# Performance work log

Hardware: AMD Instinct MI355X
Metric: run time of the kernel (lower is better)

The kernel has to match this reference:

```python
import jax, jax.numpy as jnp
import numpy as np

B, T, C, H = 2, 2048, 1024, 16
D = C // H  # head_dim = 64

def setup_inputs() -> dict:
    key = jax.random.key(0)
    ks = jax.random.split(key, 5)
    x = jax.random.normal(ks[0], (B, T, C), dtype=jnp.float32)
    Wqkv = jax.random.normal(ks[1], (C, 3 * C), dtype=jnp.float32) * 0.02
    bqkv = jnp.zeros((3 * C,), dtype=jnp.float32)
    Wout = jax.random.normal(ks[2], (C, C), dtype=jnp.float32) * 0.02
    bout = jnp.zeros((C,), dtype=jnp.float32)
    return {"x": x, "Wqkv": Wqkv, "bqkv": bqkv, "Wout": Wout, "bout": bout}

def reference(x, Wqkv, bqkv, Wout, bout):
    Bb, Tt, Cc = x.shape
    qkv = x @ Wqkv + bqkv                       # [B,T,3C]
    qkv = qkv.reshape(Bb, Tt, 3, H, D)
    qkv = jnp.transpose(qkv, (2, 0, 3, 1, 4))   # [3,B,H,T,D]
    q, k, v = qkv[0], qkv[1], qkv[2]
    scale = 1.0 / np.sqrt(D).astype(np.float32)
    scores = jnp.einsum('bhqd,bhkd->bhqk', q, k) * scale  # [B,H,T,T]
    causal = jnp.tril(jnp.ones((Tt, Tt), dtype=bool))
    scores = jnp.where(causal[None, None, :, :], scores, jnp.float32(-jnp.inf))
    attn = jax.nn.softmax(scores, axis=-1)
    out = jnp.einsum('bhqk,bhkd->bhqd', attn, v)          # [B,H,T,D]
    out = jnp.transpose(out, (0, 2, 1, 3)).reshape(Bb, Tt, Cc)
    return out @ Wout + bout
```

## Files before the change

### kernel.cpp

```cpp
#include <hip/hip_runtime.h>

#define Bc 2
#define Tc 2048
#define Cc 1024
#define Hc 16
#define Dc 64
#define Mtot (Bc*Tc)
#define Kdim Cc
#define N1 (3*Cc)
#define N2 Cc

typedef __attribute__((ext_vector_type(8))) short short8;
typedef __attribute__((ext_vector_type(4))) float float4v;

__device__ __forceinline__ unsigned short f2bf(float f) {
  unsigned int u = __builtin_bit_cast(unsigned int, f);
  u += 0x7FFFu + ((u >> 16) & 1u);
  return (unsigned short)(u >> 16);
}

__device__ __forceinline__ unsigned int pk_bf16(float a, float b) {
#if __has_builtin(__builtin_amdgcn_cvt_pk_bf16_f32)
  typedef __attribute__((ext_vector_type(2))) __bf16 bf16x2;
  bf16x2 v = __builtin_amdgcn_cvt_pk_bf16_f32(a, b);
  return __builtin_bit_cast(unsigned int, v);
#else
  return (unsigned int)f2bf(a) | ((unsigned int)f2bf(b) << 16);
#endif
}

__device__ __forceinline__ void gl2lds16(const unsigned short* g, unsigned short* l) {
  __builtin_amdgcn_global_load_lds((const __attribute__((address_space(1))) void*)g,
                                   (__attribute__((address_space(3))) void*)l, 16, 0, 0);
}

__global__ __launch_bounds__(256) void k_cvt_x(const float* __restrict__ x,
                                               unsigned short* __restrict__ xb, int n4) {
  int i = blockIdx.x * 256 + threadIdx.x;
  if (i >= n4) return;
  float4 v = ((const float4*)x)[i];
  uint2 o;
  o.x = pk_bf16(v.x, v.y);
  o.y = pk_bf16(v.z, v.w);
  ((uint2*)xb)[i] = o;
}

__global__ __launch_bounds__(256) void k_cvt_wT(const float* __restrict__ w,
                                                unsigned short* __restrict__ wT,
                                                int K, int N) {
  __shared__ float tile[32][33];
  int n0 = blockIdx.x * 32, k0 = blockIdx.y * 32;
  int tx = threadIdx.x & 31, ty = threadIdx.x >> 5;
  for (int i = 0; i < 4; ++i)
    tile[ty + 8*i][tx] = w[(size_t)(k0 + ty + 8*i) * N + n0 + tx];
  __syncthreads();
  for (int i = 0; i < 4; ++i)
    wT[(size_t)(n0 + ty + 8*i) * K + k0 + tx] = f2bf(tile[tx][ty + 8*i]);
}

__device__ __forceinline__ void gemm_mainloop(const unsigned short* __restrict__ A,
                                              const unsigned short* __restrict__ BT,
                                              int m0, int n0,
                                              unsigned short* As, unsigned short* Bs,
                                              float4v acc[4][4]) {
  const int tid = threadIdx.x;
  const int w = tid >> 6, lane = tid & 63;
  const int ln = lane & 15, qd = lane >> 4;
  const int wm = w >> 1, wn = w & 1;
  const int c0 = tid, c1 = tid + 256;
  const int row0 = c0 >> 2, ko0 = (c0 & 3) * 8;
  const int row1 = c1 >> 2, ko1 = (c1 & 3) * 8;
  for (int kk = 0; kk < Kdim; kk += 32) {
    __syncthreads();
    gl2lds16(A  + (size_t)(m0 + row0) * Kdim + kk + ko0, As + c0 * 8);
    gl2lds16(A  + (size_t)(m0 + row1) * Kdim + kk + ko1, As + c1 * 8);
    gl2lds16(BT + (size_t)(n0 + row0) * Kdim + kk + ko0, Bs + c0 * 8);
    gl2lds16(BT + (size_t)(n0 + row1) * Kdim + kk + ko1, Bs + c1 * 8);
    __syncthreads();
    short8 af[4], bf[4];
    for (int i = 0; i < 4; ++i)
      af[i] = *(const short8*)(As + (wm*64 + i*16 + ln) * 32 + qd*8);
    for (int j = 0; j < 4; ++j)
      bf[j] = *(const short8*)(Bs + (wn*64 + j*16 + ln) * 32 + qd*8);
    for (int i = 0; i < 4; ++i)
      for (int j = 0; j < 4; ++j)
        acc[i][j] = __builtin_amdgcn_mfma_f32_16x16x32_bf16(af[i], bf[j], acc[i][j], 0, 0, 0);
  }
}

__global__ __launch_bounds__(256) void k_gemm_qkv(const unsigned short* __restrict__ A,
                                                  const unsigned short* __restrict__ BT,
                                                  const float* __restrict__ bias,
                                                  unsigned short* __restrict__ qkv) {
  __shared__ alignas(16) unsigned short smem[64*136 + 64];
  unsigned short* As = smem;
  unsigned short* Bs = smem + 4096;
  const int m0 = blockIdx.y * 128, n0 = blockIdx.x * 128;
  const float4v zero4 = {0.f, 0.f, 0.f, 0.f};
  float4v acc[4][4];
  for (int i = 0; i < 4; ++i) for (int j = 0; j < 4; ++j) acc[i][j] = zero4;
  gemm_mainloop(A, BT, m0, n0, As, Bs, acc);
  const int tid = threadIdx.x;
  const int w = tid >> 6, lane = tid & 63;
  const int ln = lane & 15, qd = lane >> 4;
  const int wm = w >> 1, wn = w & 1;
  const int s = n0 >> 10;
  if (s < 2) {
    const float scale = (s == 0) ? 0.125f : 1.0f;
    for (int i = 0; i < 4; ++i) {
      int mbase = m0 + wm*64 + i*16 + qd*4;
      for (int j = 0; j < 4; ++j) {
        int ncol = n0 + wn*64 + j*16 + ln;
        float bv = bias[ncol];
        int rem = ncol & 1023;
        int h = rem >> 6, d = rem & 63;
        for (int r = 0; r < 4; ++r) {
          int m = mbase + r;
          int b = m >> 11, t = m & 2047;
          float val = (acc[i][j][r] + bv) * scale;
          qkv[((((size_t)s*Bc + b)*Hc + h)*Tc + t)*Dc + d] = f2bf(val);
        }
      }
    }
  } else {
    unsigned short* vbase = qkv + (size_t)2*Bc*Hc*Tc*Dc;
    const int b = m0 >> 11, t0 = m0 & 2047;
    const int h0 = (n0 & 1023) >> 6;
    for (int p = 0; p < 2; ++p) {
      __syncthreads();
      if (wn == p) {
        for (int i = 0; i < 4; ++i) {
          int tl = wm*64 + i*16 + qd*4;
          for (int j = 0; j < 4; ++j) {
            int dl = j*16 + ln;
            float bv = bias[n0 + p*64 + dl];
            uint2 pk;
            pk.x = pk_bf16(acc[i][j][0] + bv, acc[i][j][1] + bv);
            pk.y = pk_bf16(acc[i][j][2] + bv, acc[i][j][3] + bv);
            *(uint2*)(smem + dl*136 + tl) = pk;
          }
        }
      }
      __syncthreads();
      for (int ii = 0; ii < 4; ++ii) {
        int idx = tid + 256*ii;
        int row = idx >> 4, c16 = idx & 15;
        int4 v = *(const int4*)(smem + row*136 + c16*8);
        *(int4*)(vbase + (((size_t)b*Hc + h0 + p)*Dc + row)*Tc + t0 + c16*8) = v;
      }
    }
  }
}

__global__ __launch_bounds__(256) void k_gemm_out(const unsigned short* __restrict__ A,
                                                  const unsigned short* __restrict__ BT,
                                                  const float* __restrict__ bias,
                                                  float* __restrict__ out) {
  __shared__ alignas(16) unsigned short As[64*32];
  __shared__ alignas(16) unsigned short Bs[128*32];
  const int m0 = blockIdx.y * 64, n0 = blockIdx.x * 128;
  const int tid = threadIdx.x;
  const int w = tid >> 6, lane = tid & 63;
  const int ln = lane & 15, qd = lane >> 4;
  const int wm = w >> 1, wn = w & 1;
  const int arow = tid >> 2, ako = (tid & 3) * 8;
  const int c0 = tid, c1 = tid + 256;
  const int brow0 = c0 >> 2, bko0 = (c0 & 3) * 8;
  const int brow1 = c1 >> 2, bko1 = (c1 & 3) * 8;
  const float4v zero4 = {0.f, 0.f, 0.f, 0.f};
  float4v acc[2][4];
  for (int i = 0; i < 2; ++i) for (int j = 0; j < 4; ++j) acc[i][j] = zero4;
  for (int kk = 0; kk < Kdim; kk += 32) {
    __syncthreads();
    gl2lds16(A  + (size_t)(m0 + arow)  * Kdim + kk + ako,  As + tid * 8);
    gl2lds16(BT + (size_t)(n0 + brow0) * Kdim + kk + bko0, Bs + c0 * 8);
    gl2lds16(BT + (size_t)(n0 + brow1) * Kdim + kk + bko1, Bs + c1 * 8);
    __syncthreads();
    short8 af[2], bf[4];
    for (int i = 0; i < 2; ++i)
      af[i] = *(const short8*)(As + (wm*32 + i*16 + ln) * 32 + qd*8);
    for (int j = 0; j < 4; ++j)
      bf[j] = *(const short8*)(Bs + (wn*64 + j*16 + ln) * 32 + qd*8);
    for (int i = 0; i < 2; ++i)
      for (int j = 0; j < 4; ++j)
        acc[i][j] = __builtin_amdgcn_mfma_f32_16x16x32_bf16(af[i], bf[j], acc[i][j], 0, 0, 0);
  }
  for (int i = 0; i < 2; ++i) {
    int mbase = m0 + wm*32 + i*16 + qd*4;
    for (int j = 0; j < 4; ++j) {
      int ncol = n0 + wn*64 + j*16 + ln;
      float bv = bias[ncol];
      for (int r = 0; r < 4; ++r)
        out[(size_t)(mbase + r) * N2 + ncol] = acc[i][j][r] + bv;
    }
  }
}

__device__ __forceinline__ void attn_substep(
    const unsigned short* __restrict__ Ks, const unsigned short* __restrict__ Vt,
    unsigned short* __restrict__ pw,
    const short8 qa0, const short8 qa1,
    float4v* o, float& m_i, float& l_i,
    int k0, int myq, bool mask, int ln, int qd)
{
  const float L2E = 1.44269504f;
  const float4v zero4 = {0.f, 0.f, 0.f, 0.f};
  float4v s[4];
  for (int ki = 0; ki < 4; ++ki) {
    s[ki] = zero4;
    const unsigned short* kr = Ks + (ki*16 + ln)*72;
    short8 kf0 = *(const short8*)(kr + qd*8);
    short8 kf1 = *(const short8*)(kr + 32 + qd*8);
    s[ki] = __builtin_amdgcn_mfma_f32_16x16x32_bf16(kf0, qa0, s[ki], 0, 0, 0);
    s[ki] = __builtin_amdgcn_mfma_f32_16x16x32_bf16(kf1, qa1, s[ki], 0, 0, 0);
  }
  if (mask) {
    for (int ki = 0; ki < 4; ++ki) {
      int key = k0 + ki*16 + qd*4;
      for (int r = 0; r < 4; ++r)
        if (key + r > myq) s[ki][r] = -1e30f;
    }
  }
  float mt = -1e30f;
  for (int ki = 0; ki < 4; ++ki)
    for (int r = 0; r < 4; ++r) mt = fmaxf(mt, s[ki][r]);
  mt = fmaxf(mt, __shfl_xor(mt, 16));
  mt = fmaxf(mt, __shfl_xor(mt, 32));
  float mn = fmaxf(m_i, mt);
  float al = exp2f((m_i - mn) * L2E);
  m_i = mn;
  float st = 0.f;
  for (int ki = 0; ki < 4; ++ki)
    for (int r = 0; r < 4; ++r) {
      s[ki][r] = exp2f((s[ki][r] - mn) * L2E);
      st += s[ki][r];
    }
  st += __shfl_xor(st, 16);
  st += __shfl_xor(st, 32);
  l_i = l_i * al + st;
  for (int dt = 0; dt < 4; ++dt)
    for (int r = 0; r < 4; ++r) o[dt][r] *= al;
  for (int ki = 0; ki < 4; ++ki) {
    uint2 p2;
    p2.x = pk_bf16(s[ki][0], s[ki][1]);
    p2.y = pk_bf16(s[ki][2], s[ki][3]);
    *(uint2*)(pw + ln*72 + ki*16 + qd*4) = p2;
  }
  short8 pb0 = *(const short8*)(pw + ln*72 + qd*8);
  short8 pb1 = *(const short8*)(pw + ln*72 + 32 + qd*8);
  for (int dt = 0; dt < 4; ++dt) {
    const unsigned short* vr = Vt + (dt*16 + ln)*72;
    short8 va0 = *(const short8*)(vr + qd*8);
    short8 va1 = *(const short8*)(vr + 32 + qd*8);
    o[dt] = __builtin_amdgcn_mfma_f32_16x16x32_bf16(va0, pb0, o[dt], 0, 0, 0);
    o[dt] = __builtin_amdgcn_mfma_f32_16x16x32_bf16(va1, pb1, o[dt], 0, 0, 0);
  }
}

__global__ __launch_bounds__(256) void k_attn(const unsigned short* __restrict__ qb,
                                              const unsigned short* __restrict__ kb,
                                              const unsigned short* __restrict__ vT,
                                              unsigned short* __restrict__ ob) {
  __shared__ alignas(16) unsigned short Ks[64*72];
  __shared__ alignas(16) unsigned short Vt[64*72];
  __shared__ alignas(16) unsigned short Ps[4][16*72];
  const int bh = blockIdx.x;
  const int pp = blockIdx.y;
  const int qtA = 31 - pp, qtB = pp;
  const int tid = threadIdx.x;
  const int w = tid >> 6, lane = tid & 63;
  const int ln = lane & 15, qd = lane >> 4;
  const size_t base = (size_t)bh * Tc * Dc;
  const int b = bh >> 4, h = bh & 15;
  const int srow = tid >> 3, scol = (tid & 7) * 8;
  const float4v zero4 = {0.f, 0.f, 0.f, 0.f};
  unsigned short* pw = Ps[w];

  const int myqA = qtA*64 + w*16 + ln;
  const int myqB = qtB*64 + w*16 + ln;
  const unsigned short* qrA = qb + base + (size_t)myqA * Dc;
  const unsigned short* qrB = qb + base + (size_t)myqB * Dc;
  short8 qaA0 = *(const short8*)(qrA + qd*8);
  short8 qaA1 = *(const short8*)(qrA + 32 + qd*8);
  short8 qaB0 = *(const short8*)(qrB + qd*8);
  short8 qaB1 = *(const short8*)(qrB + 32 + qd*8);
  float4v oA[4], oB[4];
  for (int dt = 0; dt < 4; ++dt) { oA[dt] = zero4; oB[dt] = zero4; }
  float mA = -1e30f, lA = 0.f, mB = -1e30f, lB = 0.f;

  int4 rk0 = *(const int4*)(kb + base + (size_t)srow * Dc + scol);
  int4 rk1 = *(const int4*)(kb + base + (size_t)(srow + 32) * Dc + scol);
  int4 rv0 = *(const int4*)(vT + base + (size_t)srow * Tc + scol);
  int4 rv1 = *(const int4*)(vT + base + (size_t)(srow + 32) * Tc + scol);

  for (int kt = 0; kt <= qtA; ++kt) {
    __syncthreads();
    *(int4*)(Ks + srow*72 + scol)      = rk0;
    *(int4*)(Ks + (srow+32)*72 + scol) = rk1;
    *(int4*)(Vt + srow*72 + scol)      = rv0;
    *(int4*)(Vt + (srow+32)*72 + scol) = rv1;
    __syncthreads();
    if (kt < qtA) {
      const int k0n = (kt + 1) * 64;
      rk0 = *(const int4*)(kb + base + (size_t)(k0n + srow) * Dc + scol);
      rk1 = *(const int4*)(kb + base + (size_t)(k0n + srow + 32) * Dc + scol);
      rv0 = *(const int4*)(vT + base + (size_t)srow * Tc + k0n + scol);
      rv1 = *(const int4*)(vT + base + (size_t)(srow + 32) * Tc + k0n + scol);
    }
    attn_substep(Ks, Vt, pw, qaA0, qaA1, oA, mA, lA, kt*64, myqA, kt == qtA, ln, qd);
    if (kt <= qtB)
      attn_substep(Ks, Vt, pw, qaB0, qaB1, oB, mB, lB, kt*64, myqB, kt == qtB, ln, qd);
  }
  float invA = 1.0f / lA, invB = 1.0f / lB;
  for (int dt = 0; dt < 4; ++dt) {
    uint2 ovA, ovB;
    ovA.x = pk_bf16(oA[dt][0] * invA, oA[dt][1] * invA);
    ovA.y = pk_bf16(oA[dt][2] * invA, oA[dt][3] * invA);
    *(uint2*)(ob + (size_t)(b*Tc + myqA)*Cc + h*Dc + dt*16 + qd*4) = ovA;
    ovB.x = pk_bf16(oB[dt][0] * invB, oB[dt][1] * invB);
    ovB.y = pk_bf16(oB[dt][2] * invB, oB[dt][3] * invB);
    *(uint2*)(ob + (size_t)(b*Tc + myqB)*Cc + h*Dc + dt*16 + qd*4) = ovB;
  }
}

extern "C" void kernel_launch(void* const* d_in, const int* in_sizes, int n_in,
                              void* d_out, int out_size, void* d_ws, size_t ws_size,
                              hipStream_t stream) {
  const float* x    = (const float*)d_in[0];
  const float* Wqkv = (const float*)d_in[1];
  const float* bqkv = (const float*)d_in[2];
  const float* Wout = (const float*)d_in[3];
  const float* bout = (const float*)d_in[4];
  float* out = (float*)d_out;

  char* ws = (char*)d_ws;
  unsigned short* xb    = (unsigned short*)ws;
  unsigned short* wqkvT = (unsigned short*)(ws + 8388608);
  unsigned short* woutT = (unsigned short*)(ws + 14680064);
  unsigned short* qkvb  = (unsigned short*)(ws + 16777216);

  k_cvt_x<<<(Mtot*Kdim/4 + 255)/256, 256, 0, stream>>>(x, xb, Mtot*Kdim/4);
  k_cvt_wT<<<dim3(N1/32, Kdim/32), 256, 0, stream>>>(Wqkv, wqkvT, Kdim, N1);
  k_cvt_wT<<<dim3(N2/32, Kdim/32), 256, 0, stream>>>(Wout, woutT, Kdim, N2);
  k_gemm_qkv<<<dim3(N1/128, Mtot/128), 256, 0, stream>>>(xb, wqkvT, bqkv, qkvb);
  k_attn<<<dim3(32, 16), 256, 0, stream>>>(qkvb, qkvb + (size_t)Bc*Hc*Tc*Dc,
                                           qkvb + (size_t)2*Bc*Hc*Tc*Dc, xb);
  k_gemm_out<<<dim3(N2/128, Mtot/64), 256, 0, stream>>>(xb, woutT, bout, out);
}
```

Baseline: 208.5 us.

## Fuse x conversion into QKV GEMM, merge weight prep, double-buffer attention K/V

Drops the separate fp32-to-bf16 conversion kernel for x. The QKV GEMM now loads fp32 x directly, converts it in registers and stores it to LDS. The two weight transpose kernels are merged into one launch. The attention kernel double-buffers its K/V LDS tiles, which removes one barrier per iteration. The trade-off is that each QKV GEMM block re-reads and re-converts fp32 x (twice the A bytes, redone for every N tile), and the A path loses the async global-to-LDS load.

```diff
diff --git a/kernel.cpp b/kernel.cpp
--- a/kernel.cpp
+++ b/kernel.cpp
@@ -34,35 +34,32 @@
                                    (__attribute__((address_space(3))) void*)l, 16, 0, 0);
 }
 
-__global__ __launch_bounds__(256) void k_cvt_x(const float* __restrict__ x,
-                                               unsigned short* __restrict__ xb, int n4) {
-  int i = blockIdx.x * 256 + threadIdx.x;
-  if (i >= n4) return;
-  float4 v = ((const float4*)x)[i];
-  uint2 o;
-  o.x = pk_bf16(v.x, v.y);
-  o.y = pk_bf16(v.z, v.w);
-  ((uint2*)xb)[i] = o;
-}
-
-__global__ __launch_bounds__(256) void k_cvt_wT(const float* __restrict__ w,
-                                                unsigned short* __restrict__ wT,
-                                                int K, int N) {
+__global__ __launch_bounds__(256) void k_prep(const float* __restrict__ wqkv,
+                                              const float* __restrict__ wout,
+                                              unsigned short* __restrict__ wqkvT,
+                                              unsigned short* __restrict__ woutT) {
   __shared__ float tile[32][33];
-  int n0 = blockIdx.x * 32, k0 = blockIdx.y * 32;
+  const int bx = blockIdx.x;
+  const float* w;  unsigned short* wT;  int N, n0;
+  if (bx < 96) { w = wqkv; wT = wqkvT; N = N1; n0 = bx * 32; }
+  else         { w = wout; wT = woutT; N = N2; n0 = (bx - 96) * 32; }
+  const int k0 = blockIdx.y * 32;
   int tx = threadIdx.x & 31, ty = threadIdx.x >> 5;
   for (int i = 0; i < 4; ++i)
     tile[ty + 8*i][tx] = w[(size_t)(k0 + ty + 8*i) * N + n0 + tx];
   __syncthreads();
   for (int i = 0; i < 4; ++i)
-    wT[(size_t)(n0 + ty + 8*i) * K + k0 + tx] = f2bf(tile[tx][ty + 8*i]);
-}
-
-__device__ __forceinline__ void gemm_mainloop(const unsigned short* __restrict__ A,
-                                              const unsigned short* __restrict__ BT,
-                                              int m0, int n0,
-                                              unsigned short* As, unsigned short* Bs,
-                                              float4v acc[4][4]) {
+    wT[(size_t)(n0 + ty + 8*i) * Kdim + k0 + tx] = f2bf(tile[tx][ty + 8*i]);
+}
+
+__global__ __launch_bounds__(256) void k_gemm_qkv(const float* __restrict__ X,
+                                                  const unsigned short* __restrict__ BT,
+                                                  const float* __restrict__ bias,
+                                                  unsigned short* __restrict__ qkv) {
+  __shared__ alignas(16) unsigned short smem[64*136 + 64];
+  unsigned short* As = smem;
+  unsigned short* Bs = smem + 4096;
+  const int m0 = blockIdx.y * 128, n0 = blockIdx.x * 128;
   const int tid = threadIdx.x;
   const int w = tid >> 6, lane = tid & 63;
   const int ln = lane & 15, qd = lane >> 4;
@@ -70,12 +67,24 @@
   const int c0 = tid, c1 = tid + 256;
   const int row0 = c0 >> 2, ko0 = (c0 & 3) * 8;
   const int row1 = c1 >> 2, ko1 = (c1 & 3) * 8;
+  const float4v zero4 = {0.f, 0.f, 0.f, 0.f};
+  float4v acc[4][4];
+  for (int i = 0; i < 4; ++i) for (int j = 0; j < 4; ++j) acc[i][j] = zero4;
   for (int kk = 0; kk < Kdim; kk += 32) {
     __syncthreads();
-    gl2lds16(A  + (size_t)(m0 + row0) * Kdim + kk + ko0, As + c0 * 8);
-    gl2lds16(A  + (size_t)(m0 + row1) * Kdim + kk + ko1, As + c1 * 8);
+    float4 a0 = *(const float4*)(X + (size_t)(m0 + row0) * Kdim + kk + ko0);
+    float4 a1 = *(const float4*)(X + (size_t)(m0 + row0) * Kdim + kk + ko0 + 4);
+    float4 a2 = *(const float4*)(X + (size_t)(m0 + row1) * Kdim + kk + ko1);
+    float4 a3 = *(const float4*)(X + (size_t)(m0 + row1) * Kdim + kk + ko1 + 4);
     gl2lds16(BT + (size_t)(n0 + row0) * Kdim + kk + ko0, Bs + c0 * 8);
     gl2lds16(BT + (size_t)(n0 + row1) * Kdim + kk + ko1, Bs + c1 * 8);
+    uint4 p0, p1;
+    p0.x = pk_bf16(a0.x, a0.y); p0.y = pk_bf16(a0.z, a0.w);
+    p0.z = pk_bf16(a1.x, a1.y); p0.w = pk_bf16(a1.z, a1.w);
+    p1.x = pk_bf16(a2.x, a2.y); p1.y = pk_bf16(a2.z, a2.w);
+    p1.z = pk_bf16(a3.x, a3.y); p1.w = pk_bf16(a3.z, a3.w);
+    *(uint4*)(As + c0 * 8) = p0;
+    *(uint4*)(As + c1 * 8) = p1;
     __syncthreads();
     short8 af[4], bf[4];
     for (int i = 0; i < 4; ++i)
@@ -86,24 +95,6 @@
       for (int j = 0; j < 4; ++j)
         acc[i][j] = __builtin_amdgcn_mfma_f32_16x16x32_bf16(af[i], bf[j], acc[i][j], 0, 0, 0);
   }
-}
-
-__global__ __launch_bounds__(256) void k_gemm_qkv(const unsigned short* __restrict__ A,
-                                                  const unsigned short* __restrict__ BT,
-                                                  const float* __restrict__ bias,
-                                                  unsigned short* __restrict__ qkv) {
-  __shared__ alignas(16) unsigned short smem[64*136 + 64];
-  unsigned short* As = smem;
-  unsigned short* Bs = smem + 4096;
-  const int m0 = blockIdx.y * 128, n0 = blockIdx.x * 128;
-  const float4v zero4 = {0.f, 0.f, 0.f, 0.f};
-  float4v acc[4][4];
-  for (int i = 0; i < 4; ++i) for (int j = 0; j < 4; ++j) acc[i][j] = zero4;
-  gemm_mainloop(A, BT, m0, n0, As, Bs, acc);
-  const int tid = threadIdx.x;
-  const int w = tid >> 6, lane = tid & 63;
-  const int ln = lane & 15, qd = lane >> 4;
-  const int wm = w >> 1, wn = w & 1;
   const int s = n0 >> 10;
   if (s < 2) {
     const float scale = (s == 0) ? 0.125f : 1.0f;
@@ -261,8 +252,8 @@
                                               const unsigned short* __restrict__ kb,
                                               const unsigned short* __restrict__ vT,
                                               unsigned short* __restrict__ ob) {
-  __shared__ alignas(16) unsigned short Ks[64*72];
-  __shared__ alignas(16) unsigned short Vt[64*72];
+  __shared__ alignas(16) unsigned short Ks[2][64*72];
+  __shared__ alignas(16) unsigned short Vt[2][64*72];
   __shared__ alignas(16) unsigned short Ps[4][16*72];
   const int bh = blockIdx.x;
   const int pp = blockIdx.y;
@@ -288,18 +279,21 @@
   for (int dt = 0; dt < 4; ++dt) { oA[dt] = zero4; oB[dt] = zero4; }
   float mA = -1e30f, lA = 0.f, mB = -1e30f, lB = 0.f;
 
-  int4 rk0 = *(const int4*)(kb + base + (size_t)srow * Dc + scol);
-  int4 rk1 = *(const int4*)(kb + base + (size_t)(srow + 32) * Dc + scol);
-  int4 rv0 = *(const int4*)(vT + base + (size_t)srow * Tc + scol);
-  int4 rv1 = *(const int4*)(vT + base + (size_t)(srow + 32) * Tc + scol);
+  {
+    int4 k0v = *(const int4*)(kb + base + (size_t)srow * Dc + scol);
+    int4 k1v = *(const int4*)(kb + base + (size_t)(srow + 32) * Dc + scol);
+    int4 v0v = *(const int4*)(vT + base + (size_t)srow * Tc + scol);
+    int4 v1v = *(const int4*)(vT + base + (size_t)(srow + 32) * Tc + scol);
+    *(int4*)(Ks[0] + srow*72 + scol)      = k0v;
+    *(int4*)(Ks[0] + (srow+32)*72 + scol) = k1v;
+    *(int4*)(Vt[0] + srow*72 + scol)      = v0v;
+    *(int4*)(Vt[0] + (srow+32)*72 + scol) = v1v;
+  }
+  __syncthreads();
 
   for (int kt = 0; kt <= qtA; ++kt) {
-    __syncthreads();
-    *(int4*)(Ks + srow*72 + scol)      = rk0;
-    *(int4*)(Ks + (srow+32)*72 + scol) = rk1;
-    *(int4*)(Vt + srow*72 + scol)      = rv0;
-    *(int4*)(Vt + (srow+32)*72 + scol) = rv1;
-    __syncthreads();
+    const int cur = kt & 1;
+    int4 rk0, rk1, rv0, rv1;
     if (kt < qtA) {
       const int k0n = (kt + 1) * 64;
       rk0 = *(const int4*)(kb + base + (size_t)(k0n + srow) * Dc + scol);
@@ -307,9 +301,17 @@
       rv0 = *(const int4*)(vT + base + (size_t)srow * Tc + k0n + scol);
       rv1 = *(const int4*)(vT + base + (size_t)(srow + 32) * Tc + k0n + scol);
     }
-    attn_substep(Ks, Vt, pw, qaA0, qaA1, oA, mA, lA, kt*64, myqA, kt == qtA, ln, qd);
+    attn_substep(Ks[cur], Vt[cur], pw, qaA0, qaA1, oA, mA, lA, kt*64, myqA, kt == qtA, ln, qd);
     if (kt <= qtB)
-      attn_substep(Ks, Vt, pw, qaB0, qaB1, oB, mB, lB, kt*64, myqB, kt == qtB, ln, qd);
+      attn_substep(Ks[cur], Vt[cur], pw, qaB0, qaB1, oB, mB, lB, kt*64, myqB, kt == qtB, ln, qd);
+    if (kt < qtA) {
+      const int nxt = cur ^ 1;
+      *(int4*)(Ks[nxt] + srow*72 + scol)      = rk0;
+      *(int4*)(Ks[nxt] + (srow+32)*72 + scol) = rk1;
+      *(int4*)(Vt[nxt] + srow*72 + scol)      = rv0;
+      *(int4*)(Vt[nxt] + (srow+32)*72 + scol) = rv1;
+      __syncthreads();
+    }
   }
   float invA = 1.0f / lA, invB = 1.0f / lB;
   for (int dt = 0; dt < 4; ++dt) {
@@ -339,10 +341,8 @@
   unsigned short* woutT = (unsigned short*)(ws + 14680064);
   unsigned short* qkvb  = (unsigned short*)(ws + 16777216);
 
-  k_cvt_x<<<(Mtot*Kdim/4 + 255)/256, 256, 0, stream>>>(x, xb, Mtot*Kdim/4);
-  k_cvt_wT<<<dim3(N1/32, Kdim/32), 256, 0, stream>>>(Wqkv, wqkvT, Kdim, N1);
-  k_cvt_wT<<<dim3(N2/32, Kdim/32), 256, 0, stream>>>(Wout, woutT, Kdim, N2);
-  k_gemm_qkv<<<dim3(N1/128, Mtot/128), 256, 0, stream>>>(xb, wqkvT, bqkv, qkvb);
+  k_prep<<<dim3(128, 32), 256, 0, stream>>>(Wqkv, Wout, wqkvT, woutT);
+  k_gemm_qkv<<<dim3(N1/128, Mtot/128), 256, 0, stream>>>(x, wqkvT, bqkv, qkvb);
   k_attn<<<dim3(32, 16), 256, 0, stream>>>(qkvb, qkvb + (size_t)Bc*Hc*Tc*Dc,
                                            qkvb + (size_t)2*Bc*Hc*Tc*Dc, xb);
   k_gemm_out<<<dim3(N2/128, Mtot/64), 256, 0, stream>>>(xb, woutT, bout, out);
```

After: 223.9 us. 7.4% more time.

## Fuse all stages into one cooperative persistent kernel with grid syncs

Applied to the files above, without the earlier changes.

Merges the conversion, QKV GEMM, attention and output GEMM kernels into a single cooperative kernel of 512 blocks that separates the phases with grid-wide syncs. It also merges the three separate conversion launches into one phase. The aim is to remove per-kernel launch overhead and tail gaps between stages. The cost is grid-sync latency, fewer blocks for the QKV GEMM (768 tiles over 512 blocks, so some blocks do two) and occupancy limits from the shared-memory union. A fallback path of four separate kernels runs when the cooperative launch is unavailable.

```diff
diff --git a/kernel.cpp b/kernel.cpp
--- a/kernel.cpp
+++ b/kernel.cpp
@@ -1,4 +1,7 @@
 #include <hip/hip_runtime.h>
+#include <hip/hip_cooperative_groups.h>
+
+namespace cg = cooperative_groups;
 
 #define Bc 2
 #define Tc 2048
@@ -34,35 +37,46 @@
                                    (__attribute__((address_space(3))) void*)l, 16, 0, 0);
 }
 
-__global__ __launch_bounds__(256) void k_cvt_x(const float* __restrict__ x,
-                                               unsigned short* __restrict__ xb, int n4) {
-  int i = blockIdx.x * 256 + threadIdx.x;
-  if (i >= n4) return;
-  float4 v = ((const float4*)x)[i];
-  uint2 o;
-  o.x = pk_bf16(v.x, v.y);
-  o.y = pk_bf16(v.z, v.w);
-  ((uint2*)xb)[i] = o;
-}
-
-__global__ __launch_bounds__(256) void k_cvt_wT(const float* __restrict__ w,
-                                                unsigned short* __restrict__ wT,
-                                                int K, int N) {
-  __shared__ float tile[32][33];
-  int n0 = blockIdx.x * 32, k0 = blockIdx.y * 32;
-  int tx = threadIdx.x & 31, ty = threadIdx.x >> 5;
-  for (int i = 0; i < 4; ++i)
-    tile[ty + 8*i][tx] = w[(size_t)(k0 + ty + 8*i) * N + n0 + tx];
-  __syncthreads();
-  for (int i = 0; i < 4; ++i)
-    wT[(size_t)(n0 + ty + 8*i) * K + k0 + tx] = f2bf(tile[tx][ty + 8*i]);
-}
-
-__device__ __forceinline__ void gemm_mainloop(const unsigned short* __restrict__ A,
-                                              const unsigned short* __restrict__ BT,
-                                              int m0, int n0,
-                                              unsigned short* As, unsigned short* Bs,
-                                              float4v acc[4][4]) {
+__device__ void prep_phase(const float* __restrict__ wqkv, const float* __restrict__ wout,
+                           const float* __restrict__ x,
+                           unsigned short* __restrict__ wqkvT,
+                           unsigned short* __restrict__ woutT,
+                           unsigned short* __restrict__ xb,
+                           unsigned short* S, int bid, int nb) {
+  float (*tile)[33] = (float(*)[33])S;
+  const int tid = threadIdx.x;
+  for (int u = bid; u < 8192; u += nb) {
+    if (u >= 4096) {
+      int idx = (u - 4096) * 256 + tid;
+      float4 v = ((const float4*)x)[idx];
+      uint2 o;
+      o.x = pk_bf16(v.x, v.y);
+      o.y = pk_bf16(v.z, v.w);
+      ((uint2*)xb)[idx] = o;
+    } else {
+      int bx = u >> 5;
+      const float* w;  unsigned short* wT;  int N, n0;
+      if (bx < 96) { w = wqkv; wT = wqkvT; N = N1; n0 = bx * 32; }
+      else         { w = wout; wT = woutT; N = N2; n0 = (bx - 96) * 32; }
+      int k0 = (u & 31) * 32;
+      int tx = tid & 31, ty = tid >> 5;
+      __syncthreads();
+      for (int i = 0; i < 4; ++i)
+        tile[ty + 8*i][tx] = w[(size_t)(k0 + ty + 8*i) * N + n0 + tx];
+      __syncthreads();
+      for (int i = 0; i < 4; ++i)
+        wT[(size_t)(n0 + ty + 8*i) * Kdim + k0 + tx] = f2bf(tile[tx][ty + 8*i]);
+    }
+  }
+}
+
+__device__ void gemm_qkv_phase(const unsigned short* __restrict__ A,
+                               const unsigned short* __restrict__ BT,
+                               const float* __restrict__ bias,
+                               unsigned short* __restrict__ qkv,
+                               unsigned short* smem, int bid, int nb) {
+  unsigned short* As = smem;
+  unsigned short* Bs = smem + 4096;
   const int tid = threadIdx.x;
   const int w = tid >> 6, lane = tid & 63;
   const int ln = lane & 15, qd = lane >> 4;
@@ -70,95 +84,211 @@
   const int c0 = tid, c1 = tid + 256;
   const int row0 = c0 >> 2, ko0 = (c0 & 3) * 8;
   const int row1 = c1 >> 2, ko1 = (c1 & 3) * 8;
-  for (int kk = 0; kk < Kdim; kk += 32) {
-    __syncthreads();
-    gl2lds16(A  + (size_t)(m0 + row0) * Kdim + kk + ko0, As + c0 * 8);
-    gl2lds16(A  + (size_t)(m0 + row1) * Kdim + kk + ko1, As + c1 * 8);
-    gl2lds16(BT + (size_t)(n0 + row0) * Kdim + kk + ko0, Bs + c0 * 8);
-    gl2lds16(BT + (size_t)(n0 + row1) * Kdim + kk + ko1, Bs + c1 * 8);
-    __syncthreads();
-    short8 af[4], bf[4];
-    for (int i = 0; i < 4; ++i)
-      af[i] = *(const short8*)(As + (wm*64 + i*16 + ln) * 32 + qd*8);
-    for (int j = 0; j < 4; ++j)
-      bf[j] = *(const short8*)(Bs + (wn*64 + j*16 + ln) * 32 + qd*8);
-    for (int i = 0; i < 4; ++i)
+  const float4v zero4 = {0.f, 0.f, 0.f, 0.f};
+  for (int t = bid; t < 768; t += nb) {
+    const int m0 = (t / 24) * 128, n0 = (t % 24) * 128;
+    float4v acc[4][4];
+    for (int i = 0; i < 4; ++i) for (int j = 0; j < 4; ++j) acc[i][j] = zero4;
+    for (int kk = 0; kk < Kdim; kk += 32) {
+      __syncthreads();
+      gl2lds16(A  + (size_t)(m0 + row0) * Kdim + kk + ko0, As + c0 * 8);
+      gl2lds16(A  + (size_t)(m0 + row1) * Kdim + kk + ko1, As + c1 * 8);
+      gl2lds16(BT + (size_t)(n0 + row0) * Kdim + kk + ko0, Bs + c0 * 8);
+      gl2lds16(BT + (size_t)(n0 + row1) * Kdim + kk + ko1, Bs + c1 * 8);
+      __syncthreads();
+      short8 af[4], bf[4];
+      for (int i = 0; i < 4; ++i)
+        af[i] = *(const short8*)(As + (wm*64 + i*16 + ln) * 32 + qd*8);
       for (int j = 0; j < 4; ++j)
-        acc[i][j] = __builtin_amdgcn_mfma_f32_16x16x32_bf16(af[i], bf[j], acc[i][j], 0, 0, 0);
-  }
-}
-
-__global__ __launch_bounds__(256) void k_gemm_qkv(const unsigned short* __restrict__ A,
-                                                  const unsigned short* __restrict__ BT,
-                                                  const float* __restrict__ bias,
-                                                  unsigned short* __restrict__ qkv) {
-  __shared__ alignas(16) unsigned short smem[64*136 + 64];
-  unsigned short* As = smem;
-  unsigned short* Bs = smem + 4096;
-  const int m0 = blockIdx.y * 128, n0 = blockIdx.x * 128;
+        bf[j] = *(const short8*)(Bs + (wn*64 + j*16 + ln) * 32 + qd*8);
+      for (int i = 0; i < 4; ++i)
+        for (int j = 0; j < 4; ++j)
+          acc[i][j] = __builtin_amdgcn_mfma_f32_16x16x32_bf16(af[i], bf[j], acc[i][j], 0, 0, 0);
+    }
+    const int s = n0 >> 10;
+    if (s < 2) {
+      const float scale = (s == 0) ? 0.125f : 1.0f;
+      for (int i = 0; i < 4; ++i) {
+        int mbase = m0 + wm*64 + i*16 + qd*4;
+        for (int j = 0; j < 4; ++j) {
+          int ncol = n0 + wn*64 + j*16 + ln;
+          float bv = bias[ncol];
+          int rem = ncol & 1023;
+          int h = rem >> 6, d = rem & 63;
+          for (int r = 0; r < 4; ++r) {
+            int m = mbase + r;
+            int b = m >> 11, tt = m & 2047;
+            float val = (acc[i][j][r] + bv) * scale;
+            qkv[((((size_t)s*Bc + b)*Hc + h)*Tc + tt)*Dc + d] = f2bf(val);
+          }
+        }
+      }
+    } else {
+      unsigned short* vbase = qkv + (size_t)2*Bc*Hc*Tc*Dc;
+      const int b = m0 >> 11, t0 = m0 & 2047;
+      const int h0 = (n0 & 1023) >> 6;
+      for (int p = 0; p < 2; ++p) {
+        __syncthreads();
+        if (wn == p) {
+          for (int i = 0; i < 4; ++i) {
+            int tl = wm*64 + i*16 + qd*4;
+            for (int j = 0; j < 4; ++j) {
+              int dl = j*16 + ln;
+              float bv = bias[n0 + p*64 + dl];
+              uint2 pk;
+              pk.x = pk_bf16(acc[i][j][0] + bv, acc[i][j][1] + bv);
+              pk.y = pk_bf16(acc[i][j][2] + bv, acc[i][j][3] + bv);
+              *(uint2*)(smem + dl*136 + tl) = pk;
+            }
+          }
+        }
+        __syncthreads();
+        for (int ii = 0; ii < 4; ++ii) {
+          int idx = tid + 256*ii;
+          int row = idx >> 4, c16 = idx & 15;
+          int4 v = *(const int4*)(smem + row*136 + c16*8);
+          *(int4*)(vbase + (((size_t)b*Hc + h0 + p)*Dc + row)*Tc + t0 + c16*8) = v;
+        }
+      }
+    }
+  }
+}
+
+__device__ __forceinline__ void attn_substep(
+    const unsigned short* __restrict__ Ks, const unsigned short* __restrict__ Vt,
+    unsigned short* __restrict__ pw,
+    const short8 qa0, const short8 qa1,
+    float4v* o, float& m_i, float& l_i,
+    int k0, int myq, bool mask, int ln, int qd)
+{
+  const float L2E = 1.44269504f;
   const float4v zero4 = {0.f, 0.f, 0.f, 0.f};
-  float4v acc[4][4];
-  for (int i = 0; i < 4; ++i) for (int j = 0; j < 4; ++j) acc[i][j] = zero4;
-  gemm_mainloop(A, BT, m0, n0, As, Bs, acc);
+  float4v s[4];
+  for (int ki = 0; ki < 4; ++ki) {
+    s[ki] = zero4;
+    const unsigned short* kr = Ks + (ki*16 + ln)*72;
+    short8 kf0 = *(const short8*)(kr + qd*8);
+    short8 kf1 = *(const short8*)(kr + 32 + qd*8);
+    s[ki] = __builtin_amdgcn_mfma_f32_16x16x32_bf16(kf0, qa0, s[ki], 0, 0, 0);
+    s[ki] = __builtin_amdgcn_mfma_f32_16x16x32_bf16(kf1, qa1, s[ki], 0, 0, 0);
+  }
+  if (mask) {
+    for (int ki = 0; ki < 4; ++ki) {
+      int key = k0 + ki*16 + qd*4;
+      for (int r = 0; r < 4; ++r)
+        if (key + r > myq) s[ki][r] = -1e30f;
+    }
+  }
+  float mt = -1e30f;
+  for (int ki = 0; ki < 4; ++ki)
+    for (int r = 0; r < 4; ++r) mt = fmaxf(mt, s[ki][r]);
+  mt = fmaxf(mt, __shfl_xor(mt, 16));
+  mt = fmaxf(mt, __shfl_xor(mt, 32));
+  float mn = fmaxf(m_i, mt);
+  float al = exp2f((m_i - mn) * L2E);
+  m_i = mn;
+  float st = 0.f;
+  for (int ki = 0; ki < 4; ++ki)
+    for (int r = 0; r < 4; ++r) {
+      s[ki][r] = exp2f((s[ki][r] - mn) * L2E);
+      st += s[ki][r];
+    }
+  st += __shfl_xor(st, 16);
+  st += __shfl_xor(st, 32);
+  l_i = l_i * al + st;
+  for (int dt = 0; dt < 4; ++dt)
+    for (int r = 0; r < 4; ++r) o[dt][r] *= al;
+  for (int ki = 0; ki < 4; ++ki) {
+    uint2 p2;
+    p2.x = pk_bf16(s[ki][0], s[ki][1]);
+    p2.y = pk_bf16(s[ki][2], s[ki][3]);
+    *(uint2*)(pw + ln*72 + ki*16 + qd*4) = p2;
+  }
+  short8 pb0 = *(const short8*)(pw + ln*72 + qd*8);
+  short8 pb1 = *(const short8*)(pw + ln*72 + 32 + qd*8);
+  for (int dt = 0; dt < 4; ++dt) {
+    const unsigned short* vr = Vt + (dt*16 + ln)*72;
+    short8 va0 = *(const short8*)(vr + qd*8);
+    short8 va1 = *(const short8*)(vr + 32 + qd*8);
+    o[dt] = __builtin_amdgcn_mfma_f32_16x16x32_bf16(va0, pb0, o[dt], 0, 0, 0);
+    o[dt] = __builtin_amdgcn_mfma_f32_16x16x32_bf16(va1, pb1, o[dt], 0, 0, 0);
+  }
+}
+
+__device__ void attn_phase(const unsigned short* __restrict__ qb,
+                           const unsigned short* __restrict__ kb,
+                           const unsigned short* __restrict__ vT,
+                           unsigned short* __restrict__ ob,
+                           unsigned short* S, int bid) {
+  unsigned short* Ks = S;
+  unsigned short* Vt = S + 4608;
+  const int bh = bid & 31;
+  const int pp = bid >> 5;
+  const int qtA = 31 - pp, qtB = pp;
   const int tid = threadIdx.x;
   const int w = tid >> 6, lane = tid & 63;
   const int ln = lane & 15, qd = lane >> 4;
-  const int wm = w >> 1, wn = w & 1;
-  const int s = n0 >> 10;
-  if (s < 2) {
-    const float scale = (s == 0) ? 0.125f : 1.0f;
-    for (int i = 0; i < 4; ++i) {
-      int mbase = m0 + wm*64 + i*16 + qd*4;
-      for (int j = 0; j < 4; ++j) {
-        int ncol = n0 + wn*64 + j*16 + ln;
-        float bv = bias[ncol];
-        int rem = ncol & 1023;
-        int h = rem >> 6, d = rem & 63;
-        for (int r = 0; r < 4; ++r) {
-          int m = mbase + r;
-          int b = m >> 11, t = m & 2047;
-          float val = (acc[i][j][r] + bv) * scale;
-          qkv[((((size_t)s*Bc + b)*Hc + h)*Tc + t)*Dc + d] = f2bf(val);
-        }
-      }
-    }
-  } else {
-    unsigned short* vbase = qkv + (size_t)2*Bc*Hc*Tc*Dc;
-    const int b = m0 >> 11, t0 = m0 & 2047;
-    const int h0 = (n0 & 1023) >> 6;
-    for (int p = 0; p < 2; ++p) {
-      __syncthreads();
-      if (wn == p) {
-        for (int i = 0; i < 4; ++i) {
-          int tl = wm*64 + i*16 + qd*4;
-          for (int j = 0; j < 4; ++j) {
-            int dl = j*16 + ln;
-            float bv = bias[n0 + p*64 + dl];
-            uint2 pk;
-            pk.x = pk_bf16(acc[i][j][0] + bv, acc[i][j][1] + bv);
-            pk.y = pk_bf16(acc[i][j][2] + bv, acc[i][j][3] + bv);
-            *(uint2*)(smem + dl*136 + tl) = pk;
-          }
-        }
-      }
-      __syncthreads();
-      for (int ii = 0; ii < 4; ++ii) {
-        int idx = tid + 256*ii;
-        int row = idx >> 4, c16 = idx & 15;
-        int4 v = *(const int4*)(smem + row*136 + c16*8);
-        *(int4*)(vbase + (((size_t)b*Hc + h0 + p)*Dc + row)*Tc + t0 + c16*8) = v;
-      }
-    }
-  }
-}
-
-__global__ __launch_bounds__(256) void k_gemm_out(const unsigned short* __restrict__ A,
-                                                  const unsigned short* __restrict__ BT,
-                                                  const float* __restrict__ bias,
-                                                  float* __restrict__ out) {
-  __shared__ alignas(16) unsigned short As[64*32];
-  __shared__ alignas(16) unsigned short Bs[128*32];
-  const int m0 = blockIdx.y * 64, n0 = blockIdx.x * 128;
+  const size_t base = (size_t)bh * Tc * Dc;
+  const int b = bh >> 4, h = bh & 15;
+  const int srow = tid >> 3, scol = (tid & 7) * 8;
+  const float4v zero4 = {0.f, 0.f, 0.f, 0.f};
+  unsigned short* pw = S + 9216 + w * 1152;
+
+  const int myqA = qtA*64 + w*16 + ln;
+  const int myqB = qtB*64 + w*16 + ln;
+  const unsigned short* qrA = qb + base + (size_t)myqA * Dc;
+  const unsigned short* qrB = qb + base + (size_t)myqB * Dc;
+  short8 qaA0 = *(const short8*)(qrA + qd*8);
+  short8 qaA1 = *(const short8*)(qrA + 32 + qd*8);
+  short8 qaB0 = *(const short8*)(qrB + qd*8);
+  short8 qaB1 = *(const short8*)(qrB + 32 + qd*8);
+  float4v oA[4], oB[4];
+  for (int dt = 0; dt < 4; ++dt) { oA[dt] = zero4; oB[dt] = zero4; }
+  float mA = -1e30f, lA = 0.f, mB = -1e30f, lB = 0.f;
+
+  int4 rk0 = *(const int4*)(kb + base + (size_t)srow * Dc + scol);
+  int4 rk1 = *(const int4*)(kb + base + (size_t)(srow + 32) * Dc + scol);
+  int4 rv0 = *(const int4*)(vT + base + (size_t)srow * Tc + scol);
+  int4 rv1 = *(const int4*)(vT + base + (size_t)(srow + 32) * Tc + scol);
+
+  for (int kt = 0; kt <= qtA; ++kt) {
+    __syncthreads();
+    *(int4*)(Ks + srow*72 + scol)      = rk0;
+    *(int4*)(Ks + (srow+32)*72 + scol) = rk1;
+    *(int4*)(Vt + srow*72 + scol)      = rv0;
+    *(int4*)(Vt + (srow+32)*72 + scol) = rv1;
+    __syncthreads();
+    if (kt < qtA) {
+      const int k0n = (kt + 1) * 64;
+      rk0 = *(const int4*)(kb + base + (size_t)(k0n + srow) * Dc + scol);
+      rk1 = *(const int4*)(kb + base + (size_t)(k0n + srow + 32) * Dc + scol);
+      rv0 = *(const int4*)(vT + base + (size_t)srow * Tc + k0n + scol);
+      rv1 = *(const int4*)(vT + base + (size_t)(srow + 32) * Tc + k0n + scol);
+    }
+    attn_substep(Ks, Vt, pw, qaA0, qaA1, oA, mA, lA, kt*64, myqA, kt == qtA, ln, qd);
+    if (kt <= qtB)
+      attn_substep(Ks, Vt, pw, qaB0, qaB1, oB, mB, lB, kt*64, myqB, kt == qtB, ln, qd);
+  }
+  float invA = 1.0f / lA, invB = 1.0f / lB;
+  for (int dt = 0; dt < 4; ++dt) {
+    uint2 ovA, ovB;
+    ovA.x = pk_bf16(oA[dt][0] * invA, oA[dt][1] * invA);
+    ovA.y = pk_bf16(oA[dt][2] * invA, oA[dt][3] * invA);
+    *(uint2*)(ob + (size_t)(b*Tc + myqA)*Cc + h*Dc + dt*16 + qd*4) = ovA;
+    ovB.x = pk_bf16(oB[dt][0] * invB, oB[dt][1] * invB);
+    ovB.y = pk_bf16(oB[dt][2] * invB, oB[dt][3] * invB);
+    *(uint2*)(ob + (size_t)(b*Tc + myqB)*Cc + h*Dc + dt*16 + qd*4) = ovB;
+  }
+}
+
+__device__ void gemm_out_phase(const unsigned short* __restrict__ A,
+                               const unsigned short* __restrict__ BT,
+                               const float* __restrict__ bias,
+                               float* __restrict__ out,
+                               unsigned short* smem, int bid) {
+  unsigned short* As = smem;
+  unsigned short* Bs = smem + 2048;
+  const int m0 = (bid >> 3) * 64, n0 = (bid & 7) * 128;
   const int tid = threadIdx.x;
   const int w = tid >> 6, lane = tid & 63;
   const int ln = lane & 15, qd = lane >> 4;
@@ -196,131 +326,45 @@
   }
 }
 
-__device__ __forceinline__ void attn_substep(
-    const unsigned short* __restrict__ Ks, const unsigned short* __restrict__ Vt,
-    unsigned short* __restrict__ pw,
-    const short8 qa0, const short8 qa1,
-    float4v* o, float& m_i, float& l_i,
-    int k0, int myq, bool mask, int ln, int qd)
-{
-  const float L2E = 1.44269504f;
-  const float4v zero4 = {0.f, 0.f, 0.f, 0.f};
-  float4v s[4];
-  for (int ki = 0; ki < 4; ++ki) {
-    s[ki] = zero4;
-    const unsigned short* kr = Ks + (ki*16 + ln)*72;
-    short8 kf0 = *(const short8*)(kr + qd*8);
-    short8 kf1 = *(const short8*)(kr + 32 + qd*8);
-    s[ki] = __builtin_amdgcn_mfma_f32_16x16x32_bf16(kf0, qa0, s[ki], 0, 0, 0);
-    s[ki] = __builtin_amdgcn_mfma_f32_16x16x32_bf16(kf1, qa1, s[ki], 0, 0, 0);
-  }
-  if (mask) {
-    for (int ki = 0; ki < 4; ++ki) {
-      int key = k0 + ki*16 + qd*4;
-      for (int r = 0; r < 4; ++r)
-        if (key + r > myq) s[ki][r] = -1e30f;
-    }
-  }
-  float mt = -1e30f;
-  for (int ki = 0; ki < 4; ++ki)
-    for (int r = 0; r < 4; ++r) mt = fmaxf(mt, s[ki][r]);
-  mt = fmaxf(mt, __shfl_xor(mt, 16));
-  mt = fmaxf(mt, __shfl_xor(mt, 32));
-  float mn = fmaxf(m_i, mt);
-  float al = exp2f((m_i - mn) * L2E);
-  m_i = mn;
-  float st = 0.f;
-  for (int ki = 0; ki < 4; ++ki)
-    for (int r = 0; r < 4; ++r) {
-      s[ki][r] = exp2f((s[ki][r] - mn) * L2E);
-      st += s[ki][r];
-    }
-  st += __shfl_xor(st, 16);
-  st += __shfl_xor(st, 32);
-  l_i = l_i * al + st;
-  for (int dt = 0; dt < 4; ++dt)
-    for (int r = 0; r < 4; ++r) o[dt][r] *= al;
-  for (int ki = 0; ki < 4; ++ki) {
-    uint2 p2;
-    p2.x = pk_bf16(s[ki][0], s[ki][1]);
-    p2.y = pk_bf16(s[ki][2], s[ki][3]);
-    *(uint2*)(pw + ln*72 + ki*16 + qd*4) = p2;
-  }
-  short8 pb0 = *(const short8*)(pw + ln*72 + qd*8);
-  short8 pb1 = *(const short8*)(pw + ln*72 + 32 + qd*8);
-  for (int dt = 0; dt < 4; ++dt) {
-    const unsigned short* vr = Vt + (dt*16 + ln)*72;
-    short8 va0 = *(const short8*)(vr + qd*8);
-    short8 va1 = *(const short8*)(vr + 32 + qd*8);
-    o[dt] = __builtin_amdgcn_mfma_f32_16x16x32_bf16(va0, pb0, o[dt], 0, 0, 0);
-    o[dt] = __builtin_amdgcn_mfma_f32_16x16x32_bf16(va1, pb1, o[dt], 0, 0, 0);
-  }
-}
-
-__global__ __launch_bounds__(256) void k_attn(const unsigned short* __restrict__ qb,
-                                              const unsigned short* __restrict__ kb,
-                                              const unsigned short* __restrict__ vT,
-                                              unsigned short* __restrict__ ob) {
-  __shared__ alignas(16) unsigned short Ks[64*72];
-  __shared__ alignas(16) unsigned short Vt[64*72];
-  __shared__ alignas(16) unsigned short Ps[4][16*72];
-  const int bh = blockIdx.x;
-  const int pp = blockIdx.y;
-  const int qtA = 31 - pp, qtB = pp;
-  const int tid = threadIdx.x;
-  const int w = tid >> 6, lane = tid & 63;
-  const int ln = lane & 15, qd = lane >> 4;
-  const size_t base = (size_t)bh * Tc * Dc;
-  const int b = bh >> 4, h = bh & 15;
-  const int srow = tid >> 3, scol = (tid & 7) * 8;
-  const float4v zero4 = {0.f, 0.f, 0.f, 0.f};
-  unsigned short* pw = Ps[w];
-
-  const int myqA = qtA*64 + w*16 + ln;
-  const int myqB = qtB*64 + w*16 + ln;
-  const unsigned short* qrA = qb + base + (size_t)myqA * Dc;
-  const unsigned short* qrB = qb + base + (size_t)myqB * Dc;
-  short8 qaA0 = *(const short8*)(qrA + qd*8);
-  short8 qaA1 = *(const short8*)(qrA + 32 + qd*8);
-  short8 qaB0 = *(const short8*)(qrB + qd*8);
-  short8 qaB1 = *(const short8*)(qrB + 32 + qd*8);
-  float4v oA[4], oB[4];
-  for (int dt = 0; dt < 4; ++dt) { oA[dt] = zero4; oB[dt] = zero4; }
-  float mA = -1e30f, lA = 0.f, mB = -1e30f, lB = 0.f;
-
-  int4 rk0 = *(const int4*)(kb + base + (size_t)srow * Dc + scol);
-  int4 rk1 = *(const int4*)(kb + base + (size_t)(srow + 32) * Dc + scol);
-  int4 rv0 = *(const int4*)(vT + base + (size_t)srow * Tc + scol);
-  int4 rv1 = *(const int4*)(vT + base + (size_t)(srow + 32) * Tc + scol);
-
-  for (int kt = 0; kt <= qtA; ++kt) {
-    __syncthreads();
-    *(int4*)(Ks + srow*72 + scol)      = rk0;
-    *(int4*)(Ks + (srow+32)*72 + scol) = rk1;
-    *(int4*)(Vt + srow*72 + scol)      = rv0;
-    *(int4*)(Vt + (srow+32)*72 + scol) = rv1;
-    __syncthreads();
-    if (kt < qtA) {
-      const int k0n = (kt + 1) * 64;
-      rk0 = *(const int4*)(kb + base + (size_t)(k0n + srow) * Dc + scol);
-      rk1 = *(const int4*)(kb + base + (size_t)(k0n + srow + 32) * Dc + scol);
-      rv0 = *(const int4*)(vT + base + (size_t)srow * Tc + k0n + scol);
-      rv1 = *(const int4*)(vT + base + (size_t)(srow + 32) * Tc + k0n + scol);
-    }
-    attn_substep(Ks, Vt, pw, qaA0, qaA1, oA, mA, lA, kt*64, myqA, kt == qtA, ln, qd);
-    if (kt <= qtB)
-      attn_substep(Ks, Vt, pw, qaB0, qaB1, oB, mB, lB, kt*64, myqB, kt == qtB, ln, qd);
-  }
-  float invA = 1.0f / lA, invB = 1.0f / lB;
-  for (int dt = 0; dt < 4; ++dt) {
-    uint2 ovA, ovB;
-    ovA.x = pk_bf16(oA[dt][0] * invA, oA[dt][1] * invA);
-    ovA.y = pk_bf16(oA[dt][2] * invA, oA[dt][3] * invA);
-    *(uint2*)(ob + (size_t)(b*Tc + myqA)*Cc + h*Dc + dt*16 + qd*4) = ovA;
-    ovB.x = pk_bf16(oB[dt][0] * invB, oB[dt][1] * invB);
-    ovB.y = pk_bf16(oB[dt][2] * invB, oB[dt][3] * invB);
-    *(uint2*)(ob + (size_t)(b*Tc + myqB)*Cc + h*Dc + dt*16 + qd*4) = ovB;
-  }
+__global__ void __launch_bounds__(256)
+k_mega(const float* __restrict__ wqkv, const float* __restrict__ wout,
+       const float* __restrict__ x, const float* __restrict__ bqkv,
+       const float* __restrict__ bout, float* __restrict__ out,
+       unsigned short* __restrict__ wqkvT, unsigned short* __restrict__ woutT,
+       unsigned short* __restrict__ xb, unsigned short* __restrict__ qkvb) {
+  __shared__ alignas(16) unsigned short S[13824];
+  cg::grid_group grid = cg::this_grid();
+  const int bid = blockIdx.x;
+
+  prep_phase(wqkv, wout, x, wqkvT, woutT, xb, S, bid, 512);
+  grid.sync();
+  gemm_qkv_phase(xb, wqkvT, bqkv, qkvb, S, bid, 512);
+  grid.sync();
+  attn_phase(qkvb, qkvb + (size_t)Bc*Hc*Tc*Dc, qkvb + (size_t)2*Bc*Hc*Tc*Dc, xb, S, bid);
+  grid.sync();
+  gemm_out_phase(xb, woutT, bout, out, S, bid);
+}
+
+__global__ __launch_bounds__(256) void k_prep_sa(const float* wqkv, const float* wout,
+                                                 const float* x, unsigned short* wqkvT,
+                                                 unsigned short* woutT, unsigned short* xb) {
+  __shared__ alignas(16) unsigned short S[2112];
+  prep_phase(wqkv, wout, x, wqkvT, woutT, xb, S, blockIdx.x, 512);
+}
+__global__ __launch_bounds__(256) void k_qkv_sa(const unsigned short* A, const unsigned short* BT,
+                                                const float* bias, unsigned short* qkv) {
+  __shared__ alignas(16) unsigned short S[8768];
+  gemm_qkv_phase(A, BT, bias, qkv, S, blockIdx.x, 768);
+}
+__global__ __launch_bounds__(256) void k_attn_sa(const unsigned short* qb, const unsigned short* kb,
+                                                 const unsigned short* vT, unsigned short* ob) {
+  __shared__ alignas(16) unsigned short S[13824];
+  attn_phase(qb, kb, vT, ob, S, blockIdx.x);
+}
+__global__ __launch_bounds__(256) void k_out_sa(const unsigned short* A, const unsigned short* BT,
+                                                const float* bias, float* out) {
+  __shared__ alignas(16) unsigned short S[6144];
+  gemm_out_phase(A, BT, bias, out, S, blockIdx.x);
 }
 
 extern "C" void kernel_launch(void* const* d_in, const int* in_sizes, int n_in,
@@ -339,11 +383,21 @@
   unsigned short* woutT = (unsigned short*)(ws + 14680064);
   unsigned short* qkvb  = (unsigned short*)(ws + 16777216);
 
-  k_cvt_x<<<(Mtot*Kdim/4 + 255)/256, 256, 0, stream>>>(x, xb, Mtot*Kdim/4);
-  k_cvt_wT<<<dim3(N1/32, Kdim/32), 256, 0, stream>>>(Wqkv, wqkvT, Kdim, N1);
-  k_cvt_wT<<<dim3(N2/32, Kdim/32), 256, 0, stream>>>(Wout, woutT, Kdim, N2);
-  k_gemm_qkv<<<dim3(N1/128, Mtot/128), 256, 0, stream>>>(xb, wqkvT, bqkv, qkvb);
-  k_attn<<<dim3(32, 16), 256, 0, stream>>>(qkvb, qkvb + (size_t)Bc*Hc*Tc*Dc,
-                                           qkvb + (size_t)2*Bc*Hc*Tc*Dc, xb);
-  k_gemm_out<<<dim3(N2/128, Mtot/64), 256, 0, stream>>>(xb, woutT, bout, out);
-}
+  int blocksPerCU = 0;
+  hipError_t qerr = hipOccupancyMaxActiveBlocksPerMultiprocessor(
+      &blocksPerCU, (const void*)k_mega, 256, 0);
+  bool coop_ok = (qerr == hipSuccess) && (blocksPerCU >= 2);
+
+  if (coop_ok) {
+    void* args[] = { (void*)&Wqkv, (void*)&Wout, (void*)&x, (void*)&bqkv, (void*)&bout,
+                     (void*)&out, (void*)&wqkvT, (void*)&woutT, (void*)&xb, (void*)&qkvb };
+    hipError_t lerr = hipLaunchCooperativeKernel((const void*)k_mega, dim3(512), dim3(256),
+                                                 args, 0, stream);
+    if (lerr == hipSuccess) return;
+  }
+  k_prep_sa<<<512, 256, 0, stream>>>(Wqkv, Wout, x, wqkvT, woutT, xb);
+  k_qkv_sa<<<768, 256, 0, stream>>>(xb, wqkvT, bqkv, qkvb);
+  k_attn_sa<<<512, 256, 0, stream>>>(qkvb, qkvb + (size_t)Bc*Hc*Tc*Dc,
+                                     qkvb + (size_t)2*Bc*Hc*Tc*Dc, xb);
+  k_out_sa<<<512, 256, 0, stream>>>(xb, woutT, bout, out);
+}
```

Result: slower. 286.8 us (+37.6%).
